# Kernel optimization log

Measured on AMD Instinct MI355X. Metric: run time of the kernel, lower is better.

Reference implementation:

```python
import jax, jax.numpy as jnp
import numpy as np

N, D, S, E, H, L = 20000, 256, 4, 320000, 5, 3
EPS = 1e-5


def _layer_norm(x, g, b):
    m = x.mean(-1, keepdims=True)
    v = ((x - m) ** 2).mean(-1, keepdims=True)
    return (x - m) * jax.lax.rsqrt(v + EPS) * g + b


def _gcn_conv(h, src, dst, w, W, b):
    # GCNConv with symmetric normalization and added self-loops (weight 1).
    loops = jnp.arange(N, dtype=src.dtype)
    s = jnp.concatenate([src, loops])
    t = jnp.concatenate([dst, loops])
    we = jnp.concatenate([w, jnp.ones((N,), h.dtype)])
    deg = jax.ops.segment_sum(we, t, num_segments=N)
    dinv = jnp.where(deg > 0, jax.lax.rsqrt(jnp.maximum(deg, EPS)), 0.0)
    norm = dinv[s] * we * dinv[t]          # [E+N]
    hW = h @ W                              # [N, D]
    msg = norm[:, None] * hW[s]             # [E+N, D] gather
    return jax.ops.segment_sum(msg, t, num_segments=N) + b  # scatter-add


def _gelu(x):
    return jax.nn.gelu(x, approximate=False)  # torch nn.GELU default (exact)


def setup_inputs() -> dict:
    key = jax.random.key(0)
    ks = jax.random.split(key, 24)
    f32 = jnp.float32
    w = lambda k, sh, s=0.05: jax.random.normal(k, sh, f32) * s
    inp = {
        "x": jax.random.normal(ks[0], (S, N, D), f32),
        "edge_src": jax.random.randint(ks[1], (E,), 0, N, jnp.int32),
        "edge_dst": jax.random.randint(ks[2], (E,), 0, N, jnp.int32),
        "edge_weight": jax.random.uniform(ks[3], (E,), f32),
        # 3 GCNConv(d, d) layers
        "gcn_W": w(ks[4], (L, D, D)),
        "gcn_b": jnp.zeros((L, D), f32),
        # 3 LayerNorm(d)
        "ln_g": jnp.ones((L, D), f32),
        "ln_b": jnp.zeros((L, D), f32),
        # nn.GRU(d, d) single layer, batch_first
        "gru_Wih": w(ks[5], (3 * D, D)),
        "gru_Whh": w(ks[6], (3 * D, D)),
        "gru_bih": jnp.zeros((3 * D,), f32),
        "gru_bhh": jnp.zeros((3 * D,), f32),
        # ForecastHead: d -> d/2 -> d/4 -> H
        "fc1_W": w(ks[7], (D // 2, D)), "fc1_b": jnp.zeros((D // 2,), f32),
        "fc2_W": w(ks[8], (D // 4, D // 2)), "fc2_b": jnp.zeros((D // 4,), f32),
        "fc3_W": w(ks[9], (H, D // 4)), "fc3_b": jnp.zeros((H,), f32),
        # DirectionHead: d -> d/4 -> H
        "dh1_W": w(ks[10], (D // 4, D)), "dh1_b": jnp.zeros((D // 4,), f32),
        "dh2_W": w(ks[11], (H, D // 4)), "dh2_b": jnp.zeros((H,), f32),
    }
    return inp


def reference(x, edge_src, edge_dst, edge_weight, gcn_W, gcn_b, ln_g, ln_b,
              gru_Wih, gru_Whh, gru_bih, gru_bhh,
              fc1_W, fc1_b, fc2_W, fc2_b, fc3_W, fc3_b,
              dh1_W, dh1_b, dh2_W, dh2_b):
    # Per-snapshot GCN stack (dropout = identity in eval). Loop over the
    # small fixed snapshot count to bound the gather/scatter intermediate.
    feats = []
    for si in range(S):
        h = x[si]
        for l in range(L):
            h = _gcn_conv(h, edge_src, edge_dst, edge_weight, gcn_W[l], gcn_b[l])
            h = _layer_norm(h, ln_g[l], ln_b[l])
            h = jax.nn.relu(h)
        feats.append(h)
    seq = jnp.stack(feats, axis=0)  # [S, N, D] (time-major for scan)

    def gru_step(h, x_t):
        gi = x_t @ gru_Wih.T + gru_bih
        gh = h @ gru_Whh.T + gru_bhh
        ir, iz, ig = jnp.split(gi, 3, axis=-1)
        hr, hz, hg = jnp.split(gh, 3, axis=-1)
        r = jax.nn.sigmoid(ir + hr)
        z = jax.nn.sigmoid(iz + hz)
        n = jnp.tanh(ig + r * hg)
        return (1.0 - z) * n + z * h, None

    h_last, _ = jax.lax.scan(gru_step, jnp.zeros((N, D), x.dtype), seq)

    f = _gelu(h_last @ fc1_W.T + fc1_b)
    f = _gelu(f @ fc2_W.T + fc2_b)
    forecast = f @ fc3_W.T + fc3_b            # [N, H]
    d = _gelu(h_last @ dh1_W.T + dh1_b)
    direction = d @ dh2_W.T + dh2_b           # [N, H]
    return forecast, direction
```

## Files before the change

kernel.cpp:

```cpp
#include <hip/hip_runtime.h>
#include <hip/hip_bf16.h>

constexpr int Nn = 20000;
constexpr int D  = 256;
constexpr int S  = 4;
constexpr int E  = 320000;
constexpr int H  = 5;
constexpr int L  = 3;

using bf16 = __hip_bfloat16;
typedef __attribute__((ext_vector_type(8))) short v8s;
typedef __attribute__((ext_vector_type(4))) float v4f;

#define GLOBAL_AS __attribute__((address_space(1)))
#define LDS_AS    __attribute__((address_space(3)))

__device__ __forceinline__ float gelu_exact(float x) {
    return 0.5f * x * (1.0f + erff(x * 0.70710678118654752440f));
}
__device__ __forceinline__ unsigned short f2bu(float f) {
    bf16 h = __float2bfloat16(f);
    return *reinterpret_cast<unsigned short*>(&h);
}
__device__ __forceinline__ float b2f(unsigned short u) {
    unsigned int v = (unsigned int)u << 16;
    return __uint_as_float(v);
}

__global__ void init_deg_cnt_kernel(float* deg, int* cnt, int n) {
    int i = blockIdx.x * blockDim.x + threadIdx.x;
    if (i < n) { deg[i] = 1.0f; cnt[i] = 0; }
}
__global__ void deg_hist_kernel(const int* __restrict__ dst, const float* __restrict__ w,
                                float* __restrict__ deg, int* __restrict__ cnt, int e) {
    int i = blockIdx.x * blockDim.x + threadIdx.x;
    if (i < e) {
        int d = dst[i];
        atomicAdd(&deg[d], w[i]);
        atomicAdd(&cnt[d], 1);
    }
}
__global__ void dinv_kernel(const float* __restrict__ deg, float* __restrict__ dinv,
                            float* __restrict__ selfnorm, int n) {
    int i = blockIdx.x * blockDim.x + threadIdx.x;
    if (i < n) {
        float dg = deg[i];
        float dv = dg > 0.0f ? rsqrtf(fmaxf(dg, 1e-5f)) : 0.0f;
        dinv[i] = dv;
        selfnorm[i] = dv * dv;
    }
}
__global__ __launch_bounds__(1024) void scan_rowptr_kernel(int* __restrict__ cnt,
                                                           int* __restrict__ rowptr, int n) {
    __shared__ int wsum[16];
    __shared__ int woff[16];
    int t = threadIdx.x;
    int wave = t >> 6, lane = t & 63;
    int chunk = (n + 1023) / 1024;
    int start = t * chunk;
    int end = start + chunk; if (end > n) end = n;
    int s = 0;
    for (int i = start; i < end; ++i) s += cnt[i];
    int incl = s;
#pragma unroll
    for (int off = 1; off < 64; off <<= 1) {
        int v = __shfl_up(incl, off);
        if (lane >= off) incl += v;
    }
    int excl = incl - s;
    if (lane == 63) wsum[wave] = incl;
    __syncthreads();
    if (t == 0) {
        int acc = 0;
        for (int i = 0; i < 16; ++i) { woff[i] = acc; acc += wsum[i]; }
        rowptr[n] = acc;
    }
    __syncthreads();
    int acc = woff[wave] + excl;
    for (int i = start; i < end; ++i) {
        rowptr[i] = acc; acc += cnt[i]; cnt[i] = 0;
    }
}
__global__ void csr_fill_kernel(const int* __restrict__ src, const int* __restrict__ dst,
                                const float* __restrict__ w, const float* __restrict__ dinv,
                                const int* __restrict__ rowptr,
                                int* __restrict__ cursor, int* __restrict__ csrc,
                                float* __restrict__ cnorm, int e) {
    int i = blockIdx.x * blockDim.x + threadIdx.x;
    if (i < e) {
        int sN = src[i], dN = dst[i];
        int pos = rowptr[dN] + atomicAdd(&cursor[dN], 1);
        csrc[pos] = sN;
        cnorm[pos] = dinv[sN] * w[i] * dinv[dN];
    }
}
constexpr int CW0 = L * D * D;
constexpr int CW1 = CW0 + 3 * D * D;
constexpr int CW2 = CW1 + 3 * D * D;
constexpr int CW3 = CW2 + 128 * 256;
constexpr int CW4 = CW3 + 64 * 128;
constexpr int CW5 = CW4 + 64 * 256;
constexpr int CW6 = CW5 + 4 * D;
__global__ void convert_weights_kernel(
    const float* __restrict__ gcn_W, const float* __restrict__ Wih,
    const float* __restrict__ Whh, const float* __restrict__ fc1W,
    const float* __restrict__ fc2W, const float* __restrict__ dh1W,
    const float* __restrict__ bih, const float* __restrict__ bhh,
    unsigned short* __restrict__ Wtb, unsigned short* __restrict__ Wihb,
    unsigned short* __restrict__ Whhb, unsigned short* __restrict__ fc1Wb,
    unsigned short* __restrict__ fc2Wb, unsigned short* __restrict__ dh1Wb,
    float* __restrict__ gbias)
{
    int i = blockIdx.x * blockDim.x + threadIdx.x;
    if (i < CW0) {
        int l = i / (D * D);
        int rem = i - l * D * D;
        int k = rem / D;
        int n = rem - k * D;
        Wtb[(size_t)l * D * D + (size_t)n * D + k] = f2bu(gcn_W[i]);
    } else if (i < CW1) { int j = i - CW0; Wihb[j]  = f2bu(Wih[j]);  }
    else if (i < CW2)   { int j = i - CW1; Whhb[j]  = f2bu(Whh[j]);  }
    else if (i < CW3)   { int j = i - CW2; fc1Wb[j] = f2bu(fc1W[j]); }
    else if (i < CW4)   { int j = i - CW3; fc2Wb[j] = f2bu(fc2W[j]); }
    else if (i < CW5)   { int j = i - CW4; dh1Wb[j] = f2bu(dh1W[j]); }
    else if (i < CW6) {
        int j = i - CW5;
        int g = j >> 8, d = j & 255;
        float v;
        if (g == 0)      v = bih[d] + bhh[d];
        else if (g == 1) v = bih[D + d] + bhh[D + d];
        else if (g == 2) v = bih[2 * D + d];
        else             v = bhh[2 * D + d];
        gbias[j] = v;
    }
}
__global__ void init_h_kernel(float* h, unsigned short* hb, int n) {
    int i = blockIdx.x * blockDim.x + threadIdx.x;
    if (i < n) { h[i] = 0.0f; hb[i] = 0; }
}
__global__ __launch_bounds__(256) void x_to_blocked_kernel(const float* __restrict__ x,
                                                           unsigned short* __restrict__ out) {
    int tid = blockIdx.x * blockDim.x + threadIdx.x;
    if (tid >= Nn * S * (D / 4)) return;
    int row = tid >> 6;
    int r64 = tid & 63;
    int s = row / Nn;
    int n = row - s * Nn;
    float4 v = ((const float4*)x)[(size_t)row * 64 + r64];
    ushort4 u;
    u.x = f2bu(v.x); u.y = f2bu(v.y); u.z = f2bu(v.z); u.w = f2bu(v.w);
    ((ushort4*)out)[((size_t)(n * 4 + s)) * 64 + r64] = u;
}

#define GBM 128
#define GBN 128
#define GBK 64
template<int OUT_MODE, int ACT>
__global__ __launch_bounds__(256) void gemm_bt_bf16_kernel(
    const unsigned short* __restrict__ A, int lda,
    const unsigned short* __restrict__ B,
    const float* __restrict__ bias, unsigned short* __restrict__ C,
    int M, int N, int K)
{
    __shared__ short As[GBM * GBK];
    __shared__ short Bs[GBN * GBK];
    int tid = threadIdx.x;
    int wave = tid >> 6, lane = tid & 63;
    int ln = lane & 15, quad = lane >> 4;
    int wr = wave >> 1, wc = wave & 1;
    int bm = blockIdx.y * GBM, bn = blockIdx.x * GBN;

    v4f acc[4][4];
#pragma unroll
    for (int i = 0; i < 4; ++i)
#pragma unroll
        for (int j = 0; j < 4; ++j)
            acc[i][j] = (v4f)(0.0f);

    int lrow = lane >> 3;
    int lcol = (lane & 7) * 8;

    for (int k0 = 0; k0 < K; k0 += GBK) {
#pragma unroll
        for (int c = 0; c < 4; ++c) {
            int seg = wave * 4 + c;
            int row = seg * 8 + lrow;
            int gm = bm + row; if (gm >= M) gm = M - 1;
            __builtin_amdgcn_global_load_lds(
                (const GLOBAL_AS unsigned int*)(A + (size_t)gm * lda + k0 + lcol),
                (LDS_AS unsigned int*)(&As[row * GBK + lcol]), 16, 0, 0);
            int gn = bn + row; if (gn >= N) gn = N - 1;
            __builtin_amdgcn_global_load_lds(
                (const GLOBAL_AS unsigned int*)(B + (size_t)gn * K + k0 + lcol),
                (LDS_AS unsigned int*)(&Bs[row * GBK + lcol]), 16, 0, 0);
        }
        __syncthreads();
#pragma unroll
        for (int ks = 0; ks < 2; ++ks) {
            v8s af[4], bfr[4];
#pragma unroll
            for (int i = 0; i < 4; ++i) {
                int row = wr * 64 + i * 16 + ln;
                af[i] = *(const v8s*)(&As[row * GBK + ks * 32 + quad * 8]);
            }
#pragma unroll
            for (int j = 0; j < 4; ++j) {
                int row = wc * 64 + j * 16 + ln;
                bfr[j] = *(const v8s*)(&Bs[row * GBK + ks * 32 + quad * 8]);
            }
#pragma unroll
            for (int i = 0; i < 4; ++i)
#pragma unroll
                for (int j = 0; j < 4; ++j)
                    acc[i][j] = __builtin_amdgcn_mfma_f32_16x16x32_bf16(af[i], bfr[j], acc[i][j], 0, 0, 0);
        }
        __syncthreads();
    }
#pragma unroll
    for (int i = 0; i < 4; ++i) {
        int gmb = bm + wr * 64 + i * 16 + quad * 4;
#pragma unroll
        for (int j = 0; j < 4; ++j) {
            int gn = bn + wc * 64 + j * 16 + ln;
            float bv = (bias && gn < N) ? bias[gn] : 0.0f;
            if (OUT_MODE == 2) {
                ushort4 u;
                u.x = f2bu(acc[i][j][0] + bv);
                u.y = f2bu(acc[i][j][1] + bv);
                u.z = f2bu(acc[i][j][2] + bv);
                u.w = f2bu(acc[i][j][3] + bv);
                int node = gmb >> 2;
                *(ushort4*)(C + ((size_t)node * D + gn) * 4) = u;
            } else {
                if (gn < N) {
#pragma unroll
                    for (int r = 0; r < 4; ++r) {
                        int gm = gmb + r;
                        if (gm < M) {
                            float v = acc[i][j][r] + bv;
                            if (ACT == 1) v = gelu_exact(v);
                            C[(size_t)gm * N + gn] = f2bu(v);
                        }
                    }
                }
            }
        }
    }
}

__global__ __launch_bounds__(256) void gru_fused_kernel(
    const unsigned short* __restrict__ feat, int fstride,
    const unsigned short* __restrict__ hbf,
    const unsigned short* __restrict__ Wihb,
    const unsigned short* __restrict__ Whhb,
    const float* __restrict__ gbias,
    float* __restrict__ h, unsigned short* __restrict__ hb, int write_f32)
{
    __shared__ short As[64 * 64];
    __shared__ short Bs[192 * 64];
    int tid = threadIdx.x;
    int wave = tid >> 6, lane = tid & 63;
    int ln = lane & 15, quad = lane >> 4;
    int wm = wave >> 1, wn = wave & 1;
    int bm = blockIdx.y * 64;
    int bn = blockIdx.x * 64;

    v4f accR[2][2], accZ[2][2], accG[2][2], accHG[2][2];
#pragma unroll
    for (int mi = 0; mi < 2; ++mi)
#pragma unroll
        for (int nj = 0; nj < 2; ++nj) {
            accR[mi][nj] = (v4f)(0.0f); accZ[mi][nj] = (v4f)(0.0f);
            accG[mi][nj] = (v4f)(0.0f); accHG[mi][nj] = (v4f)(0.0f);
        }

    int lrow = lane >> 3, lcol = (lane & 7) * 8;

    for (int phase = 0; phase < 2; ++phase) {
        const unsigned short* A = phase ? hbf : feat;
        int astr = phase ? D : fstride;
        const unsigned short* W = phase ? Whhb : Wihb;
        for (int k0 = 0; k0 < D; k0 += 64) {
#pragma unroll
            for (int c = 0; c < 2; ++c) {
                int row = wave * 16 + c * 8 + lrow;
                int gm = bm + row; if (gm >= Nn) gm = Nn - 1;
                __builtin_amdgcn_global_load_lds(
                    (const GLOBAL_AS unsigned int*)(A + (size_t)gm * astr + k0 + lcol),
                    (LDS_AS unsigned int*)(&As[row * 64 + lcol]), 16, 0, 0);
            }
#pragma unroll
            for (int c = 0; c < 6; ++c) {
                int row = wave * 48 + c * 8 + lrow;
                int g = row >> 6, dloc = row & 63;
                __builtin_amdgcn_global_load_lds(
                    (const GLOBAL_AS unsigned int*)(W + ((size_t)(g * D + bn + dloc)) * D + k0 + lcol),
                    (LDS_AS unsigned int*)(&Bs[row * 64 + lcol]), 16, 0, 0);
            }
            __syncthreads();
#pragma unroll
            for (int ks = 0; ks < 2; ++ks) {
                v8s am[2];
#pragma unroll
                for (int mi = 0; mi < 2; ++mi)
                    am[mi] = *(const v8s*)(&As[(wm * 32 + mi * 16 + ln) * 64 + ks * 32 + quad * 8]);
#pragma unroll
                for (int g = 0; g < 3; ++g) {
#pragma unroll
                    for (int nj = 0; nj < 2; ++nj) {
                        v8s bf = *(const v8s*)(&Bs[(g * 64 + wn * 32 + nj * 16 + ln) * 64 + ks * 32 + quad * 8]);
#pragma unroll
                        for (int mi = 0; mi < 2; ++mi) {
                            if (g == 0)
                                accR[mi][nj] = __builtin_amdgcn_mfma_f32_16x16x32_bf16(am[mi], bf, accR[mi][nj], 0, 0, 0);
                            else if (g == 1)
                                accZ[mi][nj] = __builtin_amdgcn_mfma_f32_16x16x32_bf16(am[mi], bf, accZ[mi][nj], 0, 0, 0);
                            else if (phase == 0)
                                accG[mi][nj] = __builtin_amdgcn_mfma_f32_16x16x32_bf16(am[mi], bf, accG[mi][nj], 0, 0, 0);
                            else
                                accHG[mi][nj] = __builtin_amdgcn_mfma_f32_16x16x32_bf16(am[mi], bf, accHG[mi][nj], 0, 0, 0);
                        }
                    }
                }
            }
            __syncthreads();
        }
    }
#pragma unroll
    for (int mi = 0; mi < 2; ++mi) {
        int gm0 = bm + wm * 32 + mi * 16 + quad * 4;
#pragma unroll
        for (int nj = 0; nj < 2; ++nj) {
            int gn = bn + wn * 32 + nj * 16 + ln;
            float vbr = gbias[gn], vbz = gbias[D + gn];
            float vbig = gbias[2 * D + gn], vbhg = gbias[3 * D + gn];
#pragma unroll
            for (int r = 0; r < 4; ++r) {
                int gm = gm0 + r;
                if (gm < Nn) {
                    float rv = 1.0f / (1.0f + expf(-(accR[mi][nj][r] + vbr)));
                    float zv = 1.0f / (1.0f + expf(-(accZ[mi][nj][r] + vbz)));
                    float nv = tanhf(accG[mi][nj][r] + vbig + rv * (accHG[mi][nj][r] + vbhg));
                    float hold = h[(size_t)gm * D + gn];
                    float hv = (1.0f - zv) * nv + zv * hold;
                    if (write_f32) h[(size_t)gm * D + gn] = hv;
                    hb[(size_t)gm * D + gn] = f2bu(hv);
                }
            }
        }
    }
}

__global__ __launch_bounds__(256) void gcn_agg_ln_relu4_kernel(
    const unsigned short* __restrict__ hWb, const int* __restrict__ rowptr,
    const int* __restrict__ csrc, const float* __restrict__ cnorm,
    const float* __restrict__ selfnorm,
    const float* __restrict__ gcn_b, const float* __restrict__ ln_g,
    const float* __restrict__ ln_b, unsigned short* __restrict__ out)
{
    int wave = threadIdx.x >> 6, lane = threadIdx.x & 63;
    int i = blockIdx.x * 4 + wave;
    const ushort4* tbl = (const ushort4*)hWb;

    float acc[4][4];
    {
        float w = selfnorm[i];
#pragma unroll
        for (int q = 0; q < 4; ++q) {
            ushort4 u = tbl[(size_t)i * D + lane + q * 64];
            acc[q][0] = w * b2f(u.x); acc[q][1] = w * b2f(u.y);
            acc[q][2] = w * b2f(u.z); acc[q][3] = w * b2f(u.w);
        }
    }
    int beg = rowptr[i], end = rowptr[i + 1];
    int p = beg;
    for (; p + 1 < end; p += 2) {
        int sA = csrc[p], sB = csrc[p + 1];
        float wA = cnorm[p], wB = cnorm[p + 1];
        ushort4 uA[4], uB[4];
#pragma unroll
        for (int q = 0; q < 4; ++q) uA[q] = tbl[(size_t)sA * D + lane + q * 64];
#pragma unroll
        for (int q = 0; q < 4; ++q) uB[q] = tbl[(size_t)sB * D + lane + q * 64];
#pragma unroll
        for (int q = 0; q < 4; ++q) {
            acc[q][0] = fmaf(wA, b2f(uA[q].x), acc[q][0]);
            acc[q][1] = fmaf(wA, b2f(uA[q].y), acc[q][1]);
            acc[q][2] = fmaf(wA, b2f(uA[q].z), acc[q][2]);
            acc[q][3] = fmaf(wA, b2f(uA[q].w), acc[q][3]);
            acc[q][0] = fmaf(wB, b2f(uB[q].x), acc[q][0]);
            acc[q][1] = fmaf(wB, b2f(uB[q].y), acc[q][1]);
            acc[q][2] = fmaf(wB, b2f(uB[q].z), acc[q][2]);
            acc[q][3] = fmaf(wB, b2f(uB[q].w), acc[q][3]);
        }
    }
    if (p < end) {
        int sA = csrc[p]; float wA = cnorm[p];
#pragma unroll
        for (int q = 0; q < 4; ++q) {
            ushort4 u = tbl[(size_t)sA * D + lane + q * 64];
            acc[q][0] = fmaf(wA, b2f(u.x), acc[q][0]);
            acc[q][1] = fmaf(wA, b2f(u.y), acc[q][1]);
            acc[q][2] = fmaf(wA, b2f(u.z), acc[q][2]);
            acc[q][3] = fmaf(wA, b2f(u.w), acc[q][3]);
        }
    }
#pragma unroll
    for (int q = 0; q < 4; ++q) {
        float bb = gcn_b[lane + q * 64];
        acc[q][0] += bb; acc[q][1] += bb; acc[q][2] += bb; acc[q][3] += bb;
    }
    float s1[4], s2[4];
#pragma unroll
    for (int s = 0; s < 4; ++s) {
        s1[s] = acc[0][s] + acc[1][s] + acc[2][s] + acc[3][s];
        s2[s] = acc[0][s] * acc[0][s] + acc[1][s] * acc[1][s]
              + acc[2][s] * acc[2][s] + acc[3][s] * acc[3][s];
    }
#pragma unroll
    for (int off = 32; off > 0; off >>= 1) {
#pragma unroll
        for (int s = 0; s < 4; ++s) {
            s1[s] += __shfl_xor(s1[s], off);
            s2[s] += __shfl_xor(s2[s], off);
        }
    }
    const float inv = 1.0f / D;
    float m[4], rr[4];
#pragma unroll
    for (int s = 0; s < 4; ++s) {
        m[s] = s1[s] * inv;
        rr[s] = rsqrtf(s2[s] * inv - m[s] * m[s] + 1e-5f);
    }
    size_t ob = (size_t)(i << 2) * D;
#pragma unroll
    for (int q = 0; q < 4; ++q) {
        int d = lane + q * 64;
        float g = ln_g[d], lb = ln_b[d];
#pragma unroll
        for (int s = 0; s < 4; ++s) {
            float y = (acc[q][s] - m[s]) * rr[s] * g + lb;
            out[ob + (size_t)s * D + d] = f2bu(fmaxf(y, 0.0f));
        }
    }
}

__global__ void head5_bf_kernel(const unsigned short* __restrict__ A,
                                const float* __restrict__ W,
                                const float* __restrict__ b, float* __restrict__ C,
                                int M, int K) {
    int idx = blockIdx.x * blockDim.x + threadIdx.x;
    if (idx >= M * H) return;
    int m = idx / H;
    int h = idx - m * H;
    const ushort4* ar = (const ushort4*)(A + (size_t)m * K);
    const float* wr = W + (size_t)h * K;
    float s = 0.0f;
    for (int k4 = 0; k4 < K / 4; ++k4) {
        ushort4 u = ar[k4];
        s = fmaf(b2f(u.x), wr[4 * k4 + 0], s);
        s = fmaf(b2f(u.y), wr[4 * k4 + 1], s);
        s = fmaf(b2f(u.z), wr[4 * k4 + 2], s);
        s = fmaf(b2f(u.w), wr[4 * k4 + 3], s);
    }
    C[idx] = s + b[h];
}

extern "C" void kernel_launch(void* const* d_in, const int* in_sizes, int n_in,
                              void* d_out, int out_size, void* d_ws, size_t ws_size,
                              hipStream_t stream)
{
    const float* x     = (const float*)d_in[0];
    const int*   esrc  = (const int*)d_in[1];
    const int*   edst  = (const int*)d_in[2];
    const float* ew    = (const float*)d_in[3];
    const float* gcn_W = (const float*)d_in[4];
    const float* gcn_b = (const float*)d_in[5];
    const float* ln_g  = (const float*)d_in[6];
    const float* ln_b  = (const float*)d_in[7];
    const float* Wih   = (const float*)d_in[8];
    const float* Whh   = (const float*)d_in[9];
    const float* bih   = (const float*)d_in[10];
    const float* bhh   = (const float*)d_in[11];
    const float* fc1W  = (const float*)d_in[12];
    const float* fc1b  = (const float*)d_in[13];
    const float* fc2W  = (const float*)d_in[14];
    const float* fc2b  = (const float*)d_in[15];
    const float* fc3W  = (const float*)d_in[16];
    const float* fc3b  = (const float*)d_in[17];
    const float* dh1W  = (const float*)d_in[18];
    const float* dh1b  = (const float*)d_in[19];
    const float* dh2W  = (const float*)d_in[20];
    const float* dh2b  = (const float*)d_in[21];

    float* out = (float*)d_out;

    char* p = (char*)d_ws;
    auto alloc = [&](size_t bytes) -> void* {
        void* r = (void*)p;
        p += (bytes + 255) & ~(size_t)255;
        return r;
    };
    float* deg      = (float*)alloc((size_t)Nn * 4);
    float* dinv     = (float*)alloc((size_t)Nn * 4);
    float* selfnorm = (float*)alloc((size_t)Nn * 4);
    int*   rowptr   = (int*)alloc((size_t)(Nn + 1) * 4);
    int*   cnt      = (int*)alloc((size_t)Nn * 4);
    int*   csrc     = (int*)alloc((size_t)E * 4);
    float* cnorm    = (float*)alloc((size_t)E * 4);
    unsigned short* Wtb   = (unsigned short*)alloc((size_t)L * D * D * 2);
    unsigned short* Wihb  = (unsigned short*)alloc((size_t)3 * D * D * 2);
    unsigned short* Whhb  = (unsigned short*)alloc((size_t)3 * D * D * 2);
    unsigned short* fc1Wb = (unsigned short*)alloc((size_t)128 * 256 * 2);
    unsigned short* fc2Wb = (unsigned short*)alloc((size_t)64 * 128 * 2);
    unsigned short* dh1Wb = (unsigned short*)alloc((size_t)64 * 256 * 2);
    float* gbias    = (float*)alloc((size_t)4 * D * 4);
    unsigned short* bufA  = (unsigned short*)alloc((size_t)Nn * S * D * 2);
    unsigned short* hWb   = (unsigned short*)alloc((size_t)Nn * D * S * 2);
    float* hgru     = (float*)alloc((size_t)Nn * D * 4);
    unsigned short* hgru_bf = (unsigned short*)alloc((size_t)Nn * D * 2);
    unsigned short* f1 = (unsigned short*)alloc((size_t)Nn * 128 * 2);
    unsigned short* f2 = (unsigned short*)alloc((size_t)Nn * 64 * 2);
    unsigned short* d1 = (unsigned short*)alloc((size_t)Nn * 64 * 2);

    auto cdiv = [](int a, int b) { return (a + b - 1) / b; };

    init_deg_cnt_kernel<<<cdiv(Nn, 256), 256, 0, stream>>>(deg, cnt, Nn);
    deg_hist_kernel<<<cdiv(E, 256), 256, 0, stream>>>(edst, ew, deg, cnt, E);
    dinv_kernel<<<cdiv(Nn, 256), 256, 0, stream>>>(deg, dinv, selfnorm, Nn);
    scan_rowptr_kernel<<<1, 1024, 0, stream>>>(cnt, rowptr, Nn);
    csr_fill_kernel<<<cdiv(E, 256), 256, 0, stream>>>(esrc, edst, ew, dinv, rowptr, cnt, csrc, cnorm, E);
    convert_weights_kernel<<<cdiv(CW6, 256), 256, 0, stream>>>(
        gcn_W, Wih, Whh, fc1W, fc2W, dh1W, bih, bhh,
        Wtb, Wihb, Whhb, fc1Wb, fc2Wb, dh1Wb, gbias);
    init_h_kernel<<<cdiv(Nn * D, 256), 256, 0, stream>>>(hgru, hgru_bf, Nn * D);
    x_to_blocked_kernel<<<cdiv(Nn * S * D / 4, 256), 256, 0, stream>>>(x, bufA);

    for (int l = 0; l < L; ++l) {
        dim3 g1(D / GBN, (Nn * S) / GBM);
        gemm_bt_bf16_kernel<2, 0><<<g1, 256, 0, stream>>>(
            bufA, D, Wtb + (size_t)l * D * D, nullptr, hWb, Nn * S, D, D);
        gcn_agg_ln_relu4_kernel<<<Nn / 4, 256, 0, stream>>>(
            hWb, rowptr, csrc, cnorm, selfnorm,
            gcn_b + (size_t)l * D, ln_g + (size_t)l * D, ln_b + (size_t)l * D, bufA);
    }

    for (int s = 0; s < S; ++s) {
        dim3 g2(D / 64, cdiv(Nn, 64));
        gru_fused_kernel<<<g2, 256, 0, stream>>>(
            bufA + (size_t)s * D, S * D, hgru_bf, Wihb, Whhb, gbias,
            hgru, hgru_bf, (s < S - 1) ? 1 : 0);
    }

    {
        dim3 gf1(1, cdiv(Nn, GBM));
        gemm_bt_bf16_kernel<1, 1><<<gf1, 256, 0, stream>>>(
            hgru_bf, D, fc1Wb, fc1b, f1, Nn, 128, 256);
        gemm_bt_bf16_kernel<1, 1><<<gf1, 256, 0, stream>>>(
            f1, 128, fc2Wb, fc2b, f2, Nn, 64, 128);
        head5_bf_kernel<<<cdiv(Nn * H, 256), 256, 0, stream>>>(f2, fc3W, fc3b, out, Nn, 64);
        gemm_bt_bf16_kernel<1, 1><<<gf1, 256, 0, stream>>>(
            hgru_bf, D, dh1Wb, dh1b, d1, Nn, 64, 256);
        head5_bf_kernel<<<cdiv(Nn * H, 256), 256, 0, stream>>>(d1, dh2W, dh2b, out + (size_t)Nn * H, Nn, 64);
    }
}
```

Before: 881.3 us.

## Split GCN aggregation into feature-chunked gather and separate LayerNorm pass

The GEMM epilogue now writes the transformed features in a chunked layout, with 8 chunks of 32 ushort4 units per node. A new gather kernel processes one chunk per block, and two half-waves split the edges and combine their sums with a shuffle. The per-chunk working set is smaller, which is meant to improve cache hit rates on the random neighbor gathers, and edge source index and norm are packed into one int2 load. In exchange the aggregate makes an extra round trip through memory in bf16 (reusing the GRU state buffer) before a separate LayerNorm/ReLU kernel, which adds traffic and a second rounding to bf16.

```diff
diff --git a/kernel.cpp b/kernel.cpp
--- a/kernel.cpp
+++ b/kernel.cpp
@@ -7,6 +7,7 @@
 constexpr int E  = 320000;
 constexpr int H  = 5;
 constexpr int L  = 3;
+constexpr int NC = 8;
 
 using bf16 = __hip_bfloat16;
 typedef __attribute__((ext_vector_type(8))) short v8s;
@@ -84,14 +85,13 @@
 __global__ void csr_fill_kernel(const int* __restrict__ src, const int* __restrict__ dst,
                                 const float* __restrict__ w, const float* __restrict__ dinv,
                                 const int* __restrict__ rowptr,
-                                int* __restrict__ cursor, int* __restrict__ csrc,
-                                float* __restrict__ cnorm, int e) {
+                                int* __restrict__ cursor, int2* __restrict__ esw, int e) {
     int i = blockIdx.x * blockDim.x + threadIdx.x;
     if (i < e) {
         int sN = src[i], dN = dst[i];
         int pos = rowptr[dN] + atomicAdd(&cursor[dN], 1);
-        csrc[pos] = sN;
-        cnorm[pos] = dinv[sN] * w[i] * dinv[dN];
+        float nrm = dinv[sN] * w[i] * dinv[dN];
+        esw[pos] = make_int2(sN, __float_as_int(nrm));
     }
 }
 constexpr int CW0 = L * D * D;
@@ -230,7 +230,8 @@
                 u.z = f2bu(acc[i][j][2] + bv);
                 u.w = f2bu(acc[i][j][3] + bv);
                 int node = gmb >> 2;
-                *(ushort4*)(C + ((size_t)node * D + gn) * 4) = u;
+                size_t u4idx = ((size_t)(gn >> 5) * Nn + node) * 32 + (gn & 31);
+                *(ushort4*)(C + u4idx * 4) = u;
             } else {
                 if (gn < N) {
 #pragma unroll
@@ -351,71 +352,71 @@
     }
 }
 
-__global__ __launch_bounds__(256) void gcn_agg_ln_relu4_kernel(
-    const unsigned short* __restrict__ hWb, const int* __restrict__ rowptr,
-    const int* __restrict__ csrc, const float* __restrict__ cnorm,
+__global__ __launch_bounds__(256) void gcn_gather_chunk_kernel(
+    const unsigned short* __restrict__ tblc,
+    const int* __restrict__ rowptr,
+    const int2* __restrict__ esw,
     const float* __restrict__ selfnorm,
+    unsigned short* __restrict__ hAgg)
+{
+    int gid = blockIdx.x;
+    int c  = gid & 7;
+    int nb = gid >> 3;
+    int wave = threadIdx.x >> 6, lane = threadIdx.x & 63;
+    int i = nb * 4 + wave;
+    int g = lane >> 5;
+    int t = lane & 31;
+    const ushort4* tbl = (const ushort4*)tblc + (size_t)c * Nn * 32;
+
+    float a0, a1, a2, a3;
+    {
+        float w = (g == 0) ? selfnorm[i] : 0.0f;
+        ushort4 u = tbl[(size_t)i * 32 + t];
+        a0 = w * b2f(u.x); a1 = w * b2f(u.y);
+        a2 = w * b2f(u.z); a3 = w * b2f(u.w);
+    }
+    int p = rowptr[i], end = rowptr[i + 1];
+    for (; p < end; p += 2) {
+        int q = p + g;
+        int qc = (q < end) ? q : p;
+        int2 e = esw[qc];
+        float w = (q < end) ? __int_as_float(e.y) : 0.0f;
+        ushort4 u = tbl[(size_t)e.x * 32 + t];
+        a0 = fmaf(w, b2f(u.x), a0);
+        a1 = fmaf(w, b2f(u.y), a1);
+        a2 = fmaf(w, b2f(u.z), a2);
+        a3 = fmaf(w, b2f(u.w), a3);
+    }
+    a0 += __shfl_xor(a0, 32);
+    a1 += __shfl_xor(a1, 32);
+    a2 += __shfl_xor(a2, 32);
+    a3 += __shfl_xor(a3, 32);
+    if (g == 0) {
+        ushort4 o;
+        o.x = f2bu(a0); o.y = f2bu(a1); o.z = f2bu(a2); o.w = f2bu(a3);
+        ((ushort4*)hAgg)[(size_t)c * Nn * 32 + (size_t)i * 32 + t] = o;
+    }
+}
+
+__global__ __launch_bounds__(256) void gcn_ln_relu_kernel(
+    const unsigned short* __restrict__ hAgg,
     const float* __restrict__ gcn_b, const float* __restrict__ ln_g,
     const float* __restrict__ ln_b, unsigned short* __restrict__ out)
 {
     int wave = threadIdx.x >> 6, lane = threadIdx.x & 63;
     int i = blockIdx.x * 4 + wave;
-    const ushort4* tbl = (const ushort4*)hWb;
-
-    float acc[4][4];
-    {
-        float w = selfnorm[i];
-#pragma unroll
-        for (int q = 0; q < 4; ++q) {
-            ushort4 u = tbl[(size_t)i * D + lane + q * 64];
-            acc[q][0] = w * b2f(u.x); acc[q][1] = w * b2f(u.y);
-            acc[q][2] = w * b2f(u.z); acc[q][3] = w * b2f(u.w);
-        }
-    }
-    int beg = rowptr[i], end = rowptr[i + 1];
-    int p = beg;
-    for (; p + 1 < end; p += 2) {
-        int sA = csrc[p], sB = csrc[p + 1];
-        float wA = cnorm[p], wB = cnorm[p + 1];
-        ushort4 uA[4], uB[4];
-#pragma unroll
-        for (int q = 0; q < 4; ++q) uA[q] = tbl[(size_t)sA * D + lane + q * 64];
-#pragma unroll
-        for (int q = 0; q < 4; ++q) uB[q] = tbl[(size_t)sB * D + lane + q * 64];
-#pragma unroll
-        for (int q = 0; q < 4; ++q) {
-            acc[q][0] = fmaf(wA, b2f(uA[q].x), acc[q][0]);
-            acc[q][1] = fmaf(wA, b2f(uA[q].y), acc[q][1]);
-            acc[q][2] = fmaf(wA, b2f(uA[q].z), acc[q][2]);
-            acc[q][3] = fmaf(wA, b2f(uA[q].w), acc[q][3]);
-            acc[q][0] = fmaf(wB, b2f(uB[q].x), acc[q][0]);
-            acc[q][1] = fmaf(wB, b2f(uB[q].y), acc[q][1]);
-            acc[q][2] = fmaf(wB, b2f(uB[q].z), acc[q][2]);
-            acc[q][3] = fmaf(wB, b2f(uB[q].w), acc[q][3]);
-        }
-    }
-    if (p < end) {
-        int sA = csrc[p]; float wA = cnorm[p];
-#pragma unroll
-        for (int q = 0; q < 4; ++q) {
-            ushort4 u = tbl[(size_t)sA * D + lane + q * 64];
-            acc[q][0] = fmaf(wA, b2f(u.x), acc[q][0]);
-            acc[q][1] = fmaf(wA, b2f(u.y), acc[q][1]);
-            acc[q][2] = fmaf(wA, b2f(u.z), acc[q][2]);
-            acc[q][3] = fmaf(wA, b2f(u.w), acc[q][3]);
-        }
-    }
-#pragma unroll
-    for (int q = 0; q < 4; ++q) {
-        float bb = gcn_b[lane + q * 64];
-        acc[q][0] += bb; acc[q][1] += bb; acc[q][2] += bb; acc[q][3] += bb;
-    }
-    float s1[4], s2[4];
-#pragma unroll
-    for (int s = 0; s < 4; ++s) {
-        s1[s] = acc[0][s] + acc[1][s] + acc[2][s] + acc[3][s];
-        s2[s] = acc[0][s] * acc[0][s] + acc[1][s] * acc[1][s]
-              + acc[2][s] * acc[2][s] + acc[3][s] * acc[3][s];
+    float v[4][4];
+    float s1[4] = {0, 0, 0, 0}, s2[4] = {0, 0, 0, 0};
+#pragma unroll
+    for (int r = 0; r < 4; ++r) {
+        int unit = lane + 64 * r;
+        int c = unit >> 5, t = unit & 31;
+        ushort4 u = ((const ushort4*)hAgg)[(size_t)c * Nn * 32 + (size_t)i * 32 + t];
+        float bb = gcn_b[unit];
+        v[r][0] = b2f(u.x) + bb; v[r][1] = b2f(u.y) + bb;
+        v[r][2] = b2f(u.z) + bb; v[r][3] = b2f(u.w) + bb;
+#pragma unroll
+        for (int s = 0; s < 4; ++s) { s1[s] += v[r][s]; s2[s] += v[r][s] * v[r][s]; }
     }
 #pragma unroll
     for (int off = 32; off > 0; off >>= 1) {
@@ -434,13 +435,13 @@
     }
     size_t ob = (size_t)(i << 2) * D;
 #pragma unroll
-    for (int q = 0; q < 4; ++q) {
-        int d = lane + q * 64;
-        float g = ln_g[d], lb = ln_b[d];
+    for (int r = 0; r < 4; ++r) {
+        int unit = lane + 64 * r;
+        float g = ln_g[unit], lb = ln_b[unit];
 #pragma unroll
         for (int s = 0; s < 4; ++s) {
-            float y = (acc[q][s] - m[s]) * rr[s] * g + lb;
-            out[ob + (size_t)s * D + d] = f2bu(fmaxf(y, 0.0f));
+            float y = (v[r][s] - m[s]) * rr[s] * g + lb;
+            out[ob + (size_t)s * D + unit] = f2bu(fmaxf(y, 0.0f));
         }
     }
 }
@@ -506,8 +507,7 @@
     float* selfnorm = (float*)alloc((size_t)Nn * 4);
     int*   rowptr   = (int*)alloc((size_t)(Nn + 1) * 4);
     int*   cnt      = (int*)alloc((size_t)Nn * 4);
-    int*   csrc     = (int*)alloc((size_t)E * 4);
-    float* cnorm    = (float*)alloc((size_t)E * 4);
+    int2*  esw      = (int2*)alloc((size_t)E * 8);
     unsigned short* Wtb   = (unsigned short*)alloc((size_t)L * D * D * 2);
     unsigned short* Wihb  = (unsigned short*)alloc((size_t)3 * D * D * 2);
     unsigned short* Whhb  = (unsigned short*)alloc((size_t)3 * D * D * 2);
@@ -522,6 +522,7 @@
     unsigned short* f1 = (unsigned short*)alloc((size_t)Nn * 128 * 2);
     unsigned short* f2 = (unsigned short*)alloc((size_t)Nn * 64 * 2);
     unsigned short* d1 = (unsigned short*)alloc((size_t)Nn * 64 * 2);
+    unsigned short* hAgg = (unsigned short*)hgru;
 
     auto cdiv = [](int a, int b) { return (a + b - 1) / b; };
 
@@ -529,21 +530,23 @@
     deg_hist_kernel<<<cdiv(E, 256), 256, 0, stream>>>(edst, ew, deg, cnt, E);
     dinv_kernel<<<cdiv(Nn, 256), 256, 0, stream>>>(deg, dinv, selfnorm, Nn);
     scan_rowptr_kernel<<<1, 1024, 0, stream>>>(cnt, rowptr, Nn);
-    csr_fill_kernel<<<cdiv(E, 256), 256, 0, stream>>>(esrc, edst, ew, dinv, rowptr, cnt, csrc, cnorm, E);
+    csr_fill_kernel<<<cdiv(E, 256), 256, 0, stream>>>(esrc, edst, ew, dinv, rowptr, cnt, esw, E);
     convert_weights_kernel<<<cdiv(CW6, 256), 256, 0, stream>>>(
         gcn_W, Wih, Whh, fc1W, fc2W, dh1W, bih, bhh,
         Wtb, Wihb, Whhb, fc1Wb, fc2Wb, dh1Wb, gbias);
-    init_h_kernel<<<cdiv(Nn * D, 256), 256, 0, stream>>>(hgru, hgru_bf, Nn * D);
     x_to_blocked_kernel<<<cdiv(Nn * S * D / 4, 256), 256, 0, stream>>>(x, bufA);
 
     for (int l = 0; l < L; ++l) {
         dim3 g1(D / GBN, (Nn * S) / GBM);
         gemm_bt_bf16_kernel<2, 0><<<g1, 256, 0, stream>>>(
             bufA, D, Wtb + (size_t)l * D * D, nullptr, hWb, Nn * S, D, D);
-        gcn_agg_ln_relu4_kernel<<<Nn / 4, 256, 0, stream>>>(
-            hWb, rowptr, csrc, cnorm, selfnorm,
-            gcn_b + (size_t)l * D, ln_g + (size_t)l * D, ln_b + (size_t)l * D, bufA);
-    }
+        gcn_gather_chunk_kernel<<<NC * (Nn / 4), 256, 0, stream>>>(
+            hWb, rowptr, esw, selfnorm, hAgg);
+        gcn_ln_relu_kernel<<<Nn / 4, 256, 0, stream>>>(
+            hAgg, gcn_b + (size_t)l * D, ln_g + (size_t)l * D, ln_b + (size_t)l * D, bufA);
+    }
+
+    init_h_kernel<<<cdiv(Nn * D, 256), 256, 0, stream>>>(hgru, hgru_bf, Nn * D);
 
     for (int s = 0; s < S; ++s) {
         dim3 g2(D / 64, cdiv(Nn, 64));
```

Result: slower. 1.054 ms (+19.6%).

## Fuse x conversion into first GEMM and merge fc1/dh1 head GEMMs

Applied to the files above, without the earlier changes.

Removes the separate x-to-bf16 blocked conversion kernel by having the first GCN GEMM read fp32 x directly, converting to bf16 and remapping rows while staging into LDS. Concatenates the fc1 and dh1 weights and biases so a single GEMM produces both head hidden layers, cutting a launch and a second read of the GRU state. The trade-off is that the A-tile staging for the first layer goes through registers instead of the direct global-to-LDS load, and the concatenated output uses an N of 192 that is not a multiple of the 128 tile.

```diff
diff --git a/kernel.cpp b/kernel.cpp
--- a/kernel.cpp
+++ b/kernel.cpp
@@ -97,19 +97,20 @@
 constexpr int CW0 = L * D * D;
 constexpr int CW1 = CW0 + 3 * D * D;
 constexpr int CW2 = CW1 + 3 * D * D;
-constexpr int CW3 = CW2 + 128 * 256;
+constexpr int CW3 = CW2 + 192 * 256;
 constexpr int CW4 = CW3 + 64 * 128;
-constexpr int CW5 = CW4 + 64 * 256;
-constexpr int CW6 = CW5 + 4 * D;
+constexpr int CW5 = CW4 + 4 * D;
+constexpr int CW6 = CW5 + 192;
 __global__ void convert_weights_kernel(
     const float* __restrict__ gcn_W, const float* __restrict__ Wih,
     const float* __restrict__ Whh, const float* __restrict__ fc1W,
     const float* __restrict__ fc2W, const float* __restrict__ dh1W,
     const float* __restrict__ bih, const float* __restrict__ bhh,
+    const float* __restrict__ fc1b, const float* __restrict__ dh1b,
     unsigned short* __restrict__ Wtb, unsigned short* __restrict__ Wihb,
-    unsigned short* __restrict__ Whhb, unsigned short* __restrict__ fc1Wb,
-    unsigned short* __restrict__ fc2Wb, unsigned short* __restrict__ dh1Wb,
-    float* __restrict__ gbias)
+    unsigned short* __restrict__ Whhb, unsigned short* __restrict__ fc1dh1Wb,
+    unsigned short* __restrict__ fc2Wb,
+    float* __restrict__ gbias, float* __restrict__ hcat)
 {
     int i = blockIdx.x * blockDim.x + threadIdx.x;
     if (i < CW0) {
@@ -118,13 +119,15 @@
         int k = rem / D;
         int n = rem - k * D;
         Wtb[(size_t)l * D * D + (size_t)n * D + k] = f2bu(gcn_W[i]);
-    } else if (i < CW1) { int j = i - CW0; Wihb[j]  = f2bu(Wih[j]);  }
-    else if (i < CW2)   { int j = i - CW1; Whhb[j]  = f2bu(Whh[j]);  }
-    else if (i < CW3)   { int j = i - CW2; fc1Wb[j] = f2bu(fc1W[j]); }
+    } else if (i < CW1) { int j = i - CW0; Wihb[j] = f2bu(Wih[j]); }
+    else if (i < CW2)   { int j = i - CW1; Whhb[j] = f2bu(Whh[j]); }
+    else if (i < CW3) {
+        int j = i - CW2;
+        fc1dh1Wb[j] = (j < 128 * 256) ? f2bu(fc1W[j]) : f2bu(dh1W[j - 128 * 256]);
+    }
     else if (i < CW4)   { int j = i - CW3; fc2Wb[j] = f2bu(fc2W[j]); }
-    else if (i < CW5)   { int j = i - CW4; dh1Wb[j] = f2bu(dh1W[j]); }
-    else if (i < CW6) {
-        int j = i - CW5;
+    else if (i < CW5) {
+        int j = i - CW4;
         int g = j >> 8, d = j & 255;
         float v;
         if (g == 0)      v = bih[d] + bhh[d];
@@ -133,29 +136,20 @@
         else             v = bhh[2 * D + d];
         gbias[j] = v;
     }
+    else if (i < CW6) {
+        int j = i - CW5;
+        hcat[j] = (j < 128) ? fc1b[j] : dh1b[j - 128];
+    }
 }
 __global__ void init_h_kernel(float* h, unsigned short* hb, int n) {
     int i = blockIdx.x * blockDim.x + threadIdx.x;
     if (i < n) { h[i] = 0.0f; hb[i] = 0; }
 }
-__global__ __launch_bounds__(256) void x_to_blocked_kernel(const float* __restrict__ x,
-                                                           unsigned short* __restrict__ out) {
-    int tid = blockIdx.x * blockDim.x + threadIdx.x;
-    if (tid >= Nn * S * (D / 4)) return;
-    int row = tid >> 6;
-    int r64 = tid & 63;
-    int s = row / Nn;
-    int n = row - s * Nn;
-    float4 v = ((const float4*)x)[(size_t)row * 64 + r64];
-    ushort4 u;
-    u.x = f2bu(v.x); u.y = f2bu(v.y); u.z = f2bu(v.z); u.w = f2bu(v.w);
-    ((ushort4*)out)[((size_t)(n * 4 + s)) * 64 + r64] = u;
-}
 
 #define GBM 128
 #define GBN 128
 #define GBK 64
-template<int OUT_MODE, int ACT>
+template<int OUT_MODE, int ACT, int XIN>
 __global__ __launch_bounds__(256) void gemm_bt_bf16_kernel(
     const unsigned short* __restrict__ A, int lda,
     const unsigned short* __restrict__ B,
@@ -186,9 +180,22 @@
             int seg = wave * 4 + c;
             int row = seg * 8 + lrow;
             int gm = bm + row; if (gm >= M) gm = M - 1;
-            __builtin_amdgcn_global_load_lds(
-                (const GLOBAL_AS unsigned int*)(A + (size_t)gm * lda + k0 + lcol),
-                (LDS_AS unsigned int*)(&As[row * GBK + lcol]), 16, 0, 0);
+            if (XIN) {
+                int xr = (gm & 3) * Nn + (gm >> 2);
+                const float* xp = (const float*)A + (size_t)xr * D + k0 + lcol;
+                float4 v0 = *(const float4*)xp;
+                float4 v1 = *(const float4*)(xp + 4);
+                v8s o;
+                o[0] = (short)f2bu(v0.x); o[1] = (short)f2bu(v0.y);
+                o[2] = (short)f2bu(v0.z); o[3] = (short)f2bu(v0.w);
+                o[4] = (short)f2bu(v1.x); o[5] = (short)f2bu(v1.y);
+                o[6] = (short)f2bu(v1.z); o[7] = (short)f2bu(v1.w);
+                *(v8s*)(&As[row * GBK + lcol]) = o;
+            } else {
+                __builtin_amdgcn_global_load_lds(
+                    (const GLOBAL_AS unsigned int*)(A + (size_t)gm * lda + k0 + lcol),
+                    (LDS_AS unsigned int*)(&As[row * GBK + lcol]), 16, 0, 0);
+            }
             int gn = bn + row; if (gn >= N) gn = N - 1;
             __builtin_amdgcn_global_load_lds(
                 (const GLOBAL_AS unsigned int*)(B + (size_t)gn * K + k0 + lcol),
@@ -445,7 +452,7 @@
     }
 }
 
-__global__ void head5_bf_kernel(const unsigned short* __restrict__ A,
+__global__ void head5_bf_kernel(const unsigned short* __restrict__ A, int lda,
                                 const float* __restrict__ W,
                                 const float* __restrict__ b, float* __restrict__ C,
                                 int M, int K) {
@@ -453,7 +460,7 @@
     if (idx >= M * H) return;
     int m = idx / H;
     int h = idx - m * H;
-    const ushort4* ar = (const ushort4*)(A + (size_t)m * K);
+    const ushort4* ar = (const ushort4*)(A + (size_t)m * lda);
     const float* wr = W + (size_t)h * K;
     float s = 0.0f;
     for (int k4 = 0; k4 < K / 4; ++k4) {
@@ -508,20 +515,19 @@
     int*   cnt      = (int*)alloc((size_t)Nn * 4);
     int*   csrc     = (int*)alloc((size_t)E * 4);
     float* cnorm    = (float*)alloc((size_t)E * 4);
-    unsigned short* Wtb   = (unsigned short*)alloc((size_t)L * D * D * 2);
-    unsigned short* Wihb  = (unsigned short*)alloc((size_t)3 * D * D * 2);
-    unsigned short* Whhb  = (unsigned short*)alloc((size_t)3 * D * D * 2);
-    unsigned short* fc1Wb = (unsigned short*)alloc((size_t)128 * 256 * 2);
-    unsigned short* fc2Wb = (unsigned short*)alloc((size_t)64 * 128 * 2);
-    unsigned short* dh1Wb = (unsigned short*)alloc((size_t)64 * 256 * 2);
+    unsigned short* Wtb      = (unsigned short*)alloc((size_t)L * D * D * 2);
+    unsigned short* Wihb     = (unsigned short*)alloc((size_t)3 * D * D * 2);
+    unsigned short* Whhb     = (unsigned short*)alloc((size_t)3 * D * D * 2);
+    unsigned short* fc1dh1Wb = (unsigned short*)alloc((size_t)192 * 256 * 2);
+    unsigned short* fc2Wb    = (unsigned short*)alloc((size_t)64 * 128 * 2);
     float* gbias    = (float*)alloc((size_t)4 * D * 4);
+    float* hcat     = (float*)alloc((size_t)192 * 4);
     unsigned short* bufA  = (unsigned short*)alloc((size_t)Nn * S * D * 2);
     unsigned short* hWb   = (unsigned short*)alloc((size_t)Nn * D * S * 2);
     float* hgru     = (float*)alloc((size_t)Nn * D * 4);
     unsigned short* hgru_bf = (unsigned short*)alloc((size_t)Nn * D * 2);
-    unsigned short* f1 = (unsigned short*)alloc((size_t)Nn * 128 * 2);
-    unsigned short* f2 = (unsigned short*)alloc((size_t)Nn * 64 * 2);
-    unsigned short* d1 = (unsigned short*)alloc((size_t)Nn * 64 * 2);
+    unsigned short* f1cat = (unsigned short*)alloc((size_t)Nn * 192 * 2);
+    unsigned short* f2    = (unsigned short*)alloc((size_t)Nn * 64 * 2);
 
     auto cdiv = [](int a, int b) { return (a + b - 1) / b; };
 
@@ -531,18 +537,24 @@
     scan_rowptr_kernel<<<1, 1024, 0, stream>>>(cnt, rowptr, Nn);
     csr_fill_kernel<<<cdiv(E, 256), 256, 0, stream>>>(esrc, edst, ew, dinv, rowptr, cnt, csrc, cnorm, E);
     convert_weights_kernel<<<cdiv(CW6, 256), 256, 0, stream>>>(
-        gcn_W, Wih, Whh, fc1W, fc2W, dh1W, bih, bhh,
-        Wtb, Wihb, Whhb, fc1Wb, fc2Wb, dh1Wb, gbias);
+        gcn_W, Wih, Whh, fc1W, fc2W, dh1W, bih, bhh, fc1b, dh1b,
+        Wtb, Wihb, Whhb, fc1dh1Wb, fc2Wb, gbias, hcat);
     init_h_kernel<<<cdiv(Nn * D, 256), 256, 0, stream>>>(hgru, hgru_bf, Nn * D);
-    x_to_blocked_kernel<<<cdiv(Nn * S * D / 4, 256), 256, 0, stream>>>(x, bufA);
-
-    for (int l = 0; l < L; ++l) {
+
+    {
         dim3 g1(D / GBN, (Nn * S) / GBM);
-        gemm_bt_bf16_kernel<2, 0><<<g1, 256, 0, stream>>>(
-            bufA, D, Wtb + (size_t)l * D * D, nullptr, hWb, Nn * S, D, D);
+        gemm_bt_bf16_kernel<2, 0, 1><<<g1, 256, 0, stream>>>(
+            (const unsigned short*)x, D, Wtb, nullptr, hWb, Nn * S, D, D);
         gcn_agg_ln_relu4_kernel<<<Nn / 4, 256, 0, stream>>>(
             hWb, rowptr, csrc, cnorm, selfnorm,
-            gcn_b + (size_t)l * D, ln_g + (size_t)l * D, ln_b + (size_t)l * D, bufA);
+            gcn_b, ln_g, ln_b, bufA);
+        for (int l = 1; l < L; ++l) {
+            gemm_bt_bf16_kernel<2, 0, 0><<<g1, 256, 0, stream>>>(
+                bufA, D, Wtb + (size_t)l * D * D, nullptr, hWb, Nn * S, D, D);
+            gcn_agg_ln_relu4_kernel<<<Nn / 4, 256, 0, stream>>>(
+                hWb, rowptr, csrc, cnorm, selfnorm,
+                gcn_b + (size_t)l * D, ln_g + (size_t)l * D, ln_b + (size_t)l * D, bufA);
+        }
     }
 
     for (int s = 0; s < S; ++s) {
@@ -553,14 +565,14 @@
     }
 
     {
-        dim3 gf1(1, cdiv(Nn, GBM));
-        gemm_bt_bf16_kernel<1, 1><<<gf1, 256, 0, stream>>>(
-            hgru_bf, D, fc1Wb, fc1b, f1, Nn, 128, 256);
-        gemm_bt_bf16_kernel<1, 1><<<gf1, 256, 0, stream>>>(
-            f1, 128, fc2Wb, fc2b, f2, Nn, 64, 128);
-        head5_bf_kernel<<<cdiv(Nn * H, 256), 256, 0, stream>>>(f2, fc3W, fc3b, out, Nn, 64);
-        gemm_bt_bf16_kernel<1, 1><<<gf1, 256, 0, stream>>>(
-            hgru_bf, D, dh1Wb, dh1b, d1, Nn, 64, 256);
-        head5_bf_kernel<<<cdiv(Nn * H, 256), 256, 0, stream>>>(d1, dh2W, dh2b, out + (size_t)Nn * H, Nn, 64);
-    }
-}
+        dim3 gf1(2, cdiv(Nn, GBM));
+        gemm_bt_bf16_kernel<1, 1, 0><<<gf1, 256, 0, stream>>>(
+            hgru_bf, D, fc1dh1Wb, hcat, f1cat, Nn, 192, 256);
+        dim3 gf2(1, cdiv(Nn, GBM));
+        gemm_bt_bf16_kernel<1, 1, 0><<<gf2, 256, 0, stream>>>(
+            f1cat, 192, fc2Wb, fc2b, f2, Nn, 64, 128);
+        head5_bf_kernel<<<cdiv(Nn * H, 256), 256, 0, stream>>>(f2, 64, fc3W, fc3b, out, Nn, 64);
+        head5_bf_kernel<<<cdiv(Nn * H, 256), 256, 0, stream>>>(f1cat + 128, 192, dh2W, dh2b,
+                                                               out + (size_t)Nn * H, Nn, 64);
+    }
+}
```

New measurement: 862.4 us. 2.2% less time.
